# Optimization experiments

Hardware: AMD Instinct MI355X
Metric: run time of the kernel (lower is better)

Reference implementation:

```python
import jax, jax.numpy as jnp
import numpy as np

SIGMA = 5.0            # isotropic, voxel_size = 1 -> sigma_voxel == sigma
TRUNCATE = 3.0         # scipy gaussian_filter default truncate used in source
LABELS = (1, 2, 3, 4, 5, 6, 7, 8)
SHAPE = (128, 128, 128)
# upper-triangle entries of the 3x3 second-moment matrix, in the source's
# sorted order: diagonal (00,11,22) first, then off-diagonals (01,12,02)
XS = np.array([0, 1, 2, 0, 1, 0])
YS = np.array([0, 1, 2, 1, 2, 2])


def _gauss_kernel(sigma):
    r = int(TRUNCATE * sigma + 0.5)
    x = np.arange(-r, r + 1, dtype=np.float32)
    k = np.exp(-0.5 * (x / sigma) ** 2)
    k /= k.sum()
    return jnp.asarray(k, dtype=jnp.float32), r


def _blur_axis(arr, kernel, r, axis):
    # separable 1D convolution along `axis` with zero ('constant', cval=0) padding
    arr = jnp.moveaxis(arr, axis, -1)
    shp = arr.shape
    x = arr.reshape(-1, 1, shp[-1])                      # (N, 1, L)
    out = jax.lax.conv_general_dilated(x, kernel.reshape(1, 1, -1), (1,), [(r, r)])
    return jnp.moveaxis(out.reshape(shp), -1, axis)


def gaussian_blur3d(arr, sigma):
    k, r = _gauss_kernel(sigma)
    for ax in (-3, -2, -1):
        arr = _blur_axis(arr, k, r, ax)
    return arr


def setup_inputs() -> dict:
    key = jax.random.key(0)
    segmentation = jax.random.randint(key, SHAPE, 0, 9, dtype=jnp.int32)
    grid = jnp.meshgrid(*(jnp.arange(s, dtype=jnp.float32) for s in SHAPE), indexing='ij')
    coords = jnp.stack(grid)                              # (3, D, H, W) world coordinates
    return {"segmentation": segmentation, "coords": coords}


def _lsd(segmentation, coords):
    xs = jnp.asarray(XS)
    ys = jnp.asarray(YS)
    acc = jnp.zeros((10,) + SHAPE, dtype=jnp.float32)
    for label in LABELS:                                  # small fixed label set
        mask = (segmentation == label).astype(jnp.float32)        # (D,H,W)
        mc = coords * mask                                        # masked coords (3,...)
        outer = mc[xs] * mc[ys]                                   # unique 2nd moments (6,...)
        stack = jnp.concatenate([mask[None], mc, outer], axis=0)  # (10, D, H, W)
        agg = gaussian_blur3d(stack, SIGMA)                       # fused: one blur for all stats
        mass = agg[0]
        denom = jnp.where(mass > 0, mass, 1.0)                    # safe; invalid voxels masked out below
        com = agg[1:4] / denom                                    # center of mass (3,...)
        # mean offset, normalized by max_distance = sigma, mapped to [0,1]
        mean_offset = ((com - coords) / SIGMA * 0.5 + 0.5) * mask
        cov = (agg[4:10] / denom - com[xs] * com[ys]) / (SIGMA * SIGMA)
        desc = jnp.concatenate([mean_offset, cov, mass[None]], axis=0)
        acc = acc + desc * mask[None]                             # descriptors[mask] += descriptor[mask]
    return jnp.clip(acc, 0.0, 1.0)


def reference(segmentation, coords):
    return _lsd(segmentation, coords)
```

## Files before the change

### kernel.cpp

```cpp
#include <hip/hip_runtime.h>
#include <hip/hip_fp16.h>
#include <math.h>


constexpr int NV = 128 * 128 * 128;
constexpr int SLICE = 128 * 128;
constexpr int R = 15;
constexpr int KL = 31;
constexpr int TS = 6;
constexpr int RSTRIDE = 160 * TS + 8;
constexpr int LCAP = 512;

struct Kw { float k0[KL]; float k1[KL]; float k2[KL]; };

__device__ __forceinline__ void fma4(float4& a, float w, const float4& b) {
    a.x = fmaf(w, b.x, a.x); a.y = fmaf(w, b.y, a.y);
    a.z = fmaf(w, b.z, a.z); a.w = fmaf(w, b.w, a.w);
}

__device__ __forceinline__ float4 load_mask4(const unsigned char* p, int lab) {
    unsigned int u = *(const unsigned int*)p;
    return make_float4(((u       ) & 255u) == (unsigned)lab ? 1.f : 0.f,
                       ((u >>  8 ) & 255u) == (unsigned)lab ? 1.f : 0.f,
                       ((u >> 16 ) & 255u) == (unsigned)lab ? 1.f : 0.f,
                       ((u >> 24 ) & 255u) == (unsigned)lab ? 1.f : 0.f);
}
__device__ __forceinline__ float4 load_mask4(const int* p, int lab) {
    int4 s = *(const int4*)p;
    return make_float4(s.x == lab ? 1.f : 0.f, s.y == lab ? 1.f : 0.f,
                       s.z == lab ? 1.f : 0.f, s.w == lab ? 1.f : 0.f);
}

__device__ __forceinline__ unsigned seg_pack4(const unsigned char* p) {
    return *(const unsigned int*)p;
}
__device__ __forceinline__ unsigned seg_pack4(const int* p) {
    int4 v = *(const int4*)p;
    return (unsigned)(v.x & 255) | ((unsigned)(v.y & 255) << 8) |
           ((unsigned)(v.z & 255) << 16) | ((unsigned)(v.w & 255) << 24);
}

__device__ __forceinline__ unsigned pack_h2(float a, float b) {
    __half2 h = __float22half2_rn(make_float2(a, b));
    return *reinterpret_cast<unsigned*>(&h);
}
__device__ __forceinline__ float h_lo(unsigned u) {
    return __half2float(__ushort_as_half((unsigned short)(u & 0xffffu)));
}
__device__ __forceinline__ float h_hi(unsigned u) {
    return __half2float(__ushort_as_half((unsigned short)(u >> 16)));
}
__device__ __forceinline__ float4 h4_to_f4(uint2 u) {
    return make_float4(h_lo(u.x), h_hi(u.x), h_lo(u.y), h_hi(u.y));
}

template <typename ST>
__global__ __launch_bounds__(256) void pass_z_t(const ST* __restrict__ seg,
                                                unsigned short* __restrict__ A,
                                                int label0, size_t a_stride,
                                                Kw kw) {
    __shared__ float kp[3][37];
    if (threadIdx.x < 37) {
        int i = threadIdx.x, j = i - 3; bool ok = (j >= 0) && (j < KL);
        kp[0][i] = ok ? kw.k0[j] : 0.f;
        kp[1][i] = ok ? kw.k1[j] : 0.f;
        kp[2][i] = ok ? kw.k2[j] : 0.f;
    }
    __syncthreads();
    const int label = label0 + blockIdx.y;
    unsigned short* Ab = A + (size_t)blockIdx.y * a_stride;
    const int h = blockIdx.x, g = h & 7, l = h >> 3;
    const int tx = threadIdx.x & 31, ty = threadIdx.x >> 5;
    const int x0 = tx * 4;
    const int z0 = 16 * g + 4 * (l & 3);
    const int y  = (l >> 2) * 8 + ty;

    float4 acc[4][3];
#pragma unroll
    for (int t = 0; t < 4; ++t)
#pragma unroll
        for (int c = 0; c < 3; ++c) acc[t][c] = make_float4(0.f, 0.f, 0.f, 0.f);

    float4 cm = make_float4(0.f, 0.f, 0.f, 0.f), nm = cm;
    {
        int zz = z0 - R;
        if ((unsigned)zz < 128u)
            cm = load_mask4(seg + (zz * SLICE + y * 128 + x0), label);
        int zn = z0 + 1 - R;
        if ((unsigned)zn < 128u)
            nm = load_mask4(seg + (zn * SLICE + y * 128 + x0), label);
    }
    for (int j = 0; j < 34; ++j) {
        float4 fm = make_float4(0.f, 0.f, 0.f, 0.f);
        int zz = z0 + j + 2 - R;
        if (j < 32 && (unsigned)zz < 128u)
            fm = load_mask4(seg + (zz * SLICE + y * 128 + x0), label);
#pragma unroll
        for (int t = 0; t < 4; ++t) {
            int i = j - t + 3;
            fma4(acc[t][0], kp[0][i], cm);
            fma4(acc[t][1], kp[1][i], cm);
            fma4(acc[t][2], kp[2][i], cm);
        }
        cm = nm; nm = fm;
    }
#pragma unroll
    for (int t = 0; t < 4; ++t) {
        int base = (z0 + t) * SLICE + y * 128 + x0;
#pragma unroll
        for (int c = 0; c < 3; ++c) {
            float4 v = acc[t][c];
            uint2 pv = make_uint2(pack_h2(v.x, v.y), pack_h2(v.z, v.w));
            *reinterpret_cast<uint2*>(Ab + (size_t)c * NV + base) = pv;
        }
    }
}

__device__ __forceinline__ void conv_voxel(const unsigned short* __restrict__ Bu,
                                           int rr, int x, const Kw& kw,
                                           float o[10]) {
    const unsigned short* row = Bu + rr * RSTRIDE + (x + 1) * TS;
    float g000 = 0, g001 = 0, g002 = 0, g010 = 0, g011 = 0,
          g020 = 0, g100 = 0, g101 = 0, g110 = 0, g200 = 0;
#pragma unroll
    for (int j = 0; j < KL; ++j) {
        const unsigned* p = (const unsigned*)(row + TS * j);
        unsigned ua = p[0], ub = p[1], uc = p[2];
        float w0 = kw.k0[j], w1 = kw.k1[j], w2 = kw.k2[j];
        float b0 = h_lo(ua), b1 = h_hi(ua);
        float b2 = h_lo(ub), b3 = h_hi(ub);
        float b4 = h_lo(uc), b5 = h_hi(uc);
        g000 = fmaf(w0, b0, g000); g001 = fmaf(w1, b0, g001); g002 = fmaf(w2, b0, g002);
        g010 = fmaf(w0, b1, g010); g011 = fmaf(w1, b1, g011);
        g020 = fmaf(w0, b2, g020);
        g100 = fmaf(w0, b3, g100); g101 = fmaf(w1, b3, g101);
        g110 = fmaf(w0, b4, g110);
        g200 = fmaf(w0, b5, g200);
    }
    float mass = g000;
    float denom = (mass > 0.f) ? mass : 1.f;
    float inv = 1.f / denom;
    float p = g100 * inv, q = g010 * inv, s = g001 * inv;
    const float cs = 1.0f / 25.0f;
    o[0] = 0.5f - 0.1f * p;
    o[1] = 0.5f - 0.1f * q;
    o[2] = 0.5f - 0.1f * s;
    o[3] = (g200 * inv - p * p) * cs;
    o[4] = (g020 * inv - q * q) * cs;
    o[5] = (g002 * inv - s * s) * cs;
    o[6] = (g110 * inv - p * q) * cs;
    o[7] = (g011 * inv - q * s) * cs;
    o[8] = (g101 * inv - p * s) * cs;
    o[9] = mass;
#pragma unroll
    for (int c = 0; c < 10; ++c) o[c] = fminf(fmaxf(o[c], 0.f), 1.f);
}

__device__ __forceinline__ void do_voxel_out(const unsigned short* __restrict__ Bu,
                                             int rr, int x, int z0, int y0,
                                             float* __restrict__ out, const Kw& kw) {
    float o[10];
    conv_voxel(Bu, rr, x, kw, o);
    const int z2 = z0 + (rr >> 2), y2 = y0 + (rr & 3);
    const int v = (z2 * 128 + y2) * 128 + x;
#pragma unroll
    for (int c = 0; c < 10; ++c) out[(size_t)c * NV + v] = o[c];
}

__device__ __forceinline__ void zero_voxel(int rr, int x, int z0, int y0,
                                           float* __restrict__ out) {
    const int z2 = z0 + (rr >> 2), y2 = y0 + (rr & 3);
    const int v = (z2 * 128 + y2) * 128 + x;
#pragma unroll
    for (int c = 0; c < 10; ++c) out[(size_t)c * NV + v] = 0.f;
}

template <typename ST>
__global__ __launch_bounds__(128) void pass_yx(const unsigned short* __restrict__ A,
                                               const ST* __restrict__ seg,
                                               float* __restrict__ out,
                                               int label0, size_t a_stride,
                                               Kw kw) {
    __shared__ float4 kq4[40];
    __shared__ __align__(16) unsigned short Bu[16 * RSTRIDE];
    __shared__ unsigned short lst[LCAP];
    __shared__ int cnt;

    {
        uint4 z4 = make_uint4(0, 0, 0, 0);
        uint4* b4 = (uint4*)Bu;
        for (int i = threadIdx.x; i < 1936; i += 128) b4[i] = z4;
    }
    if (threadIdx.x < 40) {
        int i = threadIdx.x, j = i - 3; bool ok = (j >= 0) && (j < KL);
        kq4[i] = make_float4(ok ? kw.k0[j] : 0.f, ok ? kw.k1[j] : 0.f,
                             ok ? kw.k2[j] : 0.f, 0.f);
    }
    if (threadIdx.x == 0) cnt = 0;
    __syncthreads();

    const int labi = blockIdx.y;
    const int label = label0 + labi;
    const unsigned short* Ab = A + (size_t)labi * a_stride;
    const int h = blockIdx.x, g = h & 7, l = h >> 3;
    const int tx = threadIdx.x & 31, tz = threadIdx.x >> 5;
    const int x0 = tx * 4;
    const int z0 = 16 * g + 4 * (l & 3);
    const int y0 = (l >> 2) * 4;
    const int zs = (z0 + tz) * SLICE;

    const int rr_c = threadIdx.x >> 3, q0_c = threadIdx.x & 7;
    const int vrow_c = ((z0 + (rr_c >> 2)) * 128 + (y0 + (rr_c & 3))) * 128;
    unsigned pk[4];
#pragma unroll
    for (int k = 0; k < 4; ++k)
        pk[k] = seg_pack4(seg + vrow_c + 4 * (q0_c + 8 * k));

    float4 acc[6][4];
#pragma unroll
    for (int c = 0; c < 6; ++c)
#pragma unroll
        for (int t = 0; t < 4; ++t) acc[c][t] = make_float4(0.f, 0.f, 0.f, 0.f);

    uint2 c0 = make_uint2(0u, 0u), c1 = c0, c2 = c0;
    uint2 n0 = c0, n1 = c0, n2 = c0;
    {
        int yy = y0 - R;
        if ((unsigned)yy < 128u) {
            int base = zs + yy * 128 + x0;
            c0 = *(const uint2*)(Ab + base);
            c1 = *(const uint2*)(Ab + NV + base);
            c2 = *(const uint2*)(Ab + 2 * NV + base);
        }
        int yn = y0 + 1 - R;
        if ((unsigned)yn < 128u) {
            int base = zs + yn * 128 + x0;
            n0 = *(const uint2*)(Ab + base);
            n1 = *(const uint2*)(Ab + NV + base);
            n2 = *(const uint2*)(Ab + 2 * NV + base);
        }
    }
    for (int j = 0; j < 34; ++j) {
        uint2 f0 = make_uint2(0u, 0u), f1 = f0, f2 = f0;
        int yy = y0 + j + 2 - R;
        if (j < 32 && (unsigned)yy < 128u) {
            int base = zs + yy * 128 + x0;
            f0 = *(const uint2*)(Ab + base);
            f1 = *(const uint2*)(Ab + NV + base);
            f2 = *(const uint2*)(Ab + 2 * NV + base);
        }
        float4 a0 = h4_to_f4(c0), a1 = h4_to_f4(c1), a2 = h4_to_f4(c2);
#pragma unroll
        for (int t = 0; t < 4; ++t) {
            float4 wv = kq4[j + 3 - t];
            fma4(acc[0][t], wv.x, a0);
            fma4(acc[1][t], wv.y, a0);
            fma4(acc[2][t], wv.z, a0);
            fma4(acc[3][t], wv.x, a1);
            fma4(acc[4][t], wv.y, a1);
            fma4(acc[5][t], wv.x, a2);
        }
        c0 = n0; c1 = n1; c2 = n2;
        n0 = f0; n1 = f1; n2 = f2;
    }

#pragma unroll
    for (int t = 0; t < 4; ++t) {
        const int row = tz * 4 + t;
        unsigned short* rbase = Bu + row * RSTRIDE + (16 + x0) * TS;
#pragma unroll
        for (int xi = 0; xi < 4; ++xi) {
            unsigned* w32 = (unsigned*)(rbase + xi * TS);
            float v0 = (&acc[0][t].x)[xi], v1 = (&acc[1][t].x)[xi];
            float v2 = (&acc[2][t].x)[xi], v3 = (&acc[3][t].x)[xi];
            float v4 = (&acc[4][t].x)[xi], v5 = (&acc[5][t].x)[xi];
            w32[0] = pack_h2(v0, v1);
            w32[1] = pack_h2(v2, v3);
            w32[2] = pack_h2(v4, v5);
        }
    }

    {
        const int lane = threadIdx.x & 63;
        const unsigned long long below_mask = (1ull << lane) - 1ull;
#pragma unroll
        for (int k = 0; k < 4; ++k) {
            const unsigned w = pk[k];
#pragma unroll
            for (int t = 0; t < 4; ++t) {
                const int sv = (int)((w >> (8 * t)) & 255u);
                const int x = 4 * (q0_c + 8 * k) + t;
                const bool mt = (sv == label);
                const bool zt = !mt && (sv < 1 || sv > 8) &&
                                (((x & 7) + 1) == label);
                const bool pred = mt | zt;
                unsigned long long bal = __ballot(pred);
                int base = 0;
                if (lane == 0 && bal) base = atomicAdd(&cnt, (int)__popcll(bal));
                base = __shfl(base, 0);
                if (pred) {
                    int pos = base + (int)__popcll(bal & below_mask);
                    if (pos < LCAP)
                        lst[pos] = (unsigned short)((rr_c << 7) | x | (zt ? 0x8000 : 0));
                }
            }
        }
    }

    __syncthreads();

    const int total = cnt;
    if (total <= LCAP) {
        for (int e = threadIdx.x; e < total; e += 128) {
            int ent = lst[e];
            int rr = (ent >> 7) & 15, x = ent & 127;
            if (ent & 0x8000) zero_voxel(rr, x, z0, y0, out);
            else do_voxel_out(Bu, rr, x, z0, y0, out, kw);
        }
    } else {
        for (int e = threadIdx.x; e < 2048; e += 128) {
            int rr = e >> 7, x = e & 127;
            int z2 = z0 + (rr >> 2), y2 = y0 + (rr & 3);
            int sv = (int)seg[(z2 * 128 + y2) * 128 + x] & 255;
            if (sv == label)
                do_voxel_out(Bu, rr, x, z0, y0, out, kw);
            else if ((sv < 1 || sv > 8) && (((x & 7) + 1) == label))
                zero_voxel(rr, x, z0, y0, out);
        }
    }
}

__global__ __launch_bounds__(256) void seg_to_u8(const int* __restrict__ seg,
                                                 unsigned char* __restrict__ seg8) {
    const int t = blockIdx.x * 256 + threadIdx.x;
    const int4 s = ((const int4*)seg)[t];
    ((uchar4*)seg8)[t] = make_uchar4((unsigned char)s.x, (unsigned char)s.y,
                                     (unsigned char)s.z, (unsigned char)s.w);
}

extern "C" void kernel_launch(void* const* d_in, const int* in_sizes, int n_in,
                              void* d_out, int out_size, void* d_ws, size_t ws_size,
                              hipStream_t stream) {
    const int* seg = (const int*)d_in[0];
    float* out = (float*)d_out;
    unsigned short* A = (unsigned short*)d_ws;
    const size_t AVOL = (size_t)3 * NV;

    Kw kw;
    double gg[KL], S = 0.0;
    for (int j = 0; j < KL; ++j) { double d = j - R; gg[j] = exp(-0.5 * d * d / 25.0); S += gg[j]; }
    for (int j = 0; j < KL; ++j) {
        double gn = gg[j] / S, d = j - R;
        kw.k0[j] = (float)gn;
        kw.k1[j] = (float)(-d * gn);
        kw.k2[j] = (float)(d * d * gn);
    }


    const size_t need_all = 8 * AVOL * sizeof(unsigned short) + NV;
    const size_t need_one = AVOL * sizeof(unsigned short) + NV;

    if (ws_size >= need_all) {
        unsigned char* seg8 = (unsigned char*)d_ws + 8 * AVOL * sizeof(unsigned short);
        seg_to_u8<<<dim3(2048), dim3(256), 0, stream>>>(seg, seg8);
        pass_z_t<unsigned char><<<dim3(512, 8), dim3(256), 0, stream>>>(
            seg8, A, 1, AVOL, kw);
        pass_yx<unsigned char><<<dim3(1024, 8), dim3(128), 0, stream>>>(
            A, seg8, out, 1, AVOL, kw);
    } else if (ws_size >= need_one) {
        unsigned char* seg8 = (unsigned char*)d_ws + AVOL * sizeof(unsigned short);
        seg_to_u8<<<dim3(2048), dim3(256), 0, stream>>>(seg, seg8);
        for (int label = 1; label <= 8; ++label) {
            pass_z_t<unsigned char><<<dim3(512, 1), dim3(256), 0, stream>>>(
                seg8, A, label, 0, kw);
            pass_yx<unsigned char><<<dim3(1024, 1), dim3(128), 0, stream>>>(
                A, seg8, out, label, 0, kw);
        }
    } else {
        for (int label = 1; label <= 8; ++label) {
            pass_z_t<int><<<dim3(512, 1), dim3(256), 0, stream>>>(
                seg, A, label, 0, kw);
            pass_yx<int><<<dim3(1024, 1), dim3(128), 0, stream>>>(
                A, seg, out, label, 0, kw);
        }
    }
}
```

Before: 408.8 us.

## Use planar shared-memory layout and fully unrolled z/y convolutions with register weights

Changes the shared staging buffer from interleaved six-channel voxels to planar per-channel rows, so writes become packed uint2 stores and the x-convolution reads scalar halves per channel. Fully unrolls the z and y convolution loops and reads kernel weights straight from the kernel-argument struct instead of shared-memory tables, which removes the rotating register pipeline and the LDS weight loads. Shrinks the list capacity. The cost is more code, higher register pressure, and 16-bit LDS loads in the inner x loop instead of 32-bit paired loads.

```diff
diff --git a/kernel.cpp b/kernel.cpp
--- a/kernel.cpp
+++ b/kernel.cpp
@@ -7,9 +7,9 @@
 constexpr int SLICE = 128 * 128;
 constexpr int R = 15;
 constexpr int KL = 31;
-constexpr int TS = 6;
-constexpr int RSTRIDE = 160 * TS + 8;
-constexpr int LCAP = 512;
+constexpr int CSTRIDE = 160;
+constexpr int RSTRIDE = 6 * CSTRIDE + 8;
+constexpr int LCAP = 320;
 
 struct Kw { float k0[KL]; float k1[KL]; float k2[KL]; };
 
@@ -44,14 +44,14 @@
     __half2 h = __float22half2_rn(make_float2(a, b));
     return *reinterpret_cast<unsigned*>(&h);
 }
-__device__ __forceinline__ float h_lo(unsigned u) {
-    return __half2float(__ushort_as_half((unsigned short)(u & 0xffffu)));
-}
-__device__ __forceinline__ float h_hi(unsigned u) {
-    return __half2float(__ushort_as_half((unsigned short)(u >> 16)));
+__device__ __forceinline__ float hf_ld(const unsigned short* p) {
+    return __half2float(__ushort_as_half(*p));
 }
 __device__ __forceinline__ float4 h4_to_f4(uint2 u) {
-    return make_float4(h_lo(u.x), h_hi(u.x), h_lo(u.y), h_hi(u.y));
+    return make_float4(__half2float(__ushort_as_half((unsigned short)(u.x & 0xffffu))),
+                       __half2float(__ushort_as_half((unsigned short)(u.x >> 16))),
+                       __half2float(__ushort_as_half((unsigned short)(u.y & 0xffffu))),
+                       __half2float(__ushort_as_half((unsigned short)(u.y >> 16))));
 }
 
 template <typename ST>
@@ -59,14 +59,6 @@
                                                 unsigned short* __restrict__ A,
                                                 int label0, size_t a_stride,
                                                 Kw kw) {
-    __shared__ float kp[3][37];
-    if (threadIdx.x < 37) {
-        int i = threadIdx.x, j = i - 3; bool ok = (j >= 0) && (j < KL);
-        kp[0][i] = ok ? kw.k0[j] : 0.f;
-        kp[1][i] = ok ? kw.k1[j] : 0.f;
-        kp[2][i] = ok ? kw.k2[j] : 0.f;
-    }
-    __syncthreads();
     const int label = label0 + blockIdx.y;
     unsigned short* Ab = A + (size_t)blockIdx.y * a_stride;
     const int h = blockIdx.x, g = h & 7, l = h >> 3;
@@ -81,28 +73,21 @@
 #pragma unroll
         for (int c = 0; c < 3; ++c) acc[t][c] = make_float4(0.f, 0.f, 0.f, 0.f);
 
-    float4 cm = make_float4(0.f, 0.f, 0.f, 0.f), nm = cm;
-    {
-        int zz = z0 - R;
+#pragma unroll
+    for (int j = 0; j < 34; ++j) {
+        float4 m = make_float4(0.f, 0.f, 0.f, 0.f);
+        int zz = z0 + j - R;
         if ((unsigned)zz < 128u)
-            cm = load_mask4(seg + (zz * SLICE + y * 128 + x0), label);
-        int zn = z0 + 1 - R;
-        if ((unsigned)zn < 128u)
-            nm = load_mask4(seg + (zn * SLICE + y * 128 + x0), label);
-    }
-    for (int j = 0; j < 34; ++j) {
-        float4 fm = make_float4(0.f, 0.f, 0.f, 0.f);
-        int zz = z0 + j + 2 - R;
-        if (j < 32 && (unsigned)zz < 128u)
-            fm = load_mask4(seg + (zz * SLICE + y * 128 + x0), label);
+            m = load_mask4(seg + (zz * SLICE + y * 128 + x0), label);
 #pragma unroll
         for (int t = 0; t < 4; ++t) {
-            int i = j - t + 3;
-            fma4(acc[t][0], kp[0][i], cm);
-            fma4(acc[t][1], kp[1][i], cm);
-            fma4(acc[t][2], kp[2][i], cm);
-        }
-        cm = nm; nm = fm;
+            const int idx = j - t;
+            if (idx >= 0 && idx < KL) {
+                fma4(acc[t][0], kw.k0[idx], m);
+                fma4(acc[t][1], kw.k1[idx], m);
+                fma4(acc[t][2], kw.k2[idx], m);
+            }
+        }
     }
 #pragma unroll
     for (int t = 0; t < 4; ++t) {
@@ -119,17 +104,18 @@
 __device__ __forceinline__ void conv_voxel(const unsigned short* __restrict__ Bu,
                                            int rr, int x, const Kw& kw,
                                            float o[10]) {
-    const unsigned short* row = Bu + rr * RSTRIDE + (x + 1) * TS;
+    const unsigned short* row = Bu + rr * RSTRIDE + (x + 1);
     float g000 = 0, g001 = 0, g002 = 0, g010 = 0, g011 = 0,
           g020 = 0, g100 = 0, g101 = 0, g110 = 0, g200 = 0;
 #pragma unroll
     for (int j = 0; j < KL; ++j) {
-        const unsigned* p = (const unsigned*)(row + TS * j);
-        unsigned ua = p[0], ub = p[1], uc = p[2];
         float w0 = kw.k0[j], w1 = kw.k1[j], w2 = kw.k2[j];
-        float b0 = h_lo(ua), b1 = h_hi(ua);
-        float b2 = h_lo(ub), b3 = h_hi(ub);
-        float b4 = h_lo(uc), b5 = h_hi(uc);
+        float b0 = hf_ld(row + 0 * CSTRIDE + j);
+        float b1 = hf_ld(row + 1 * CSTRIDE + j);
+        float b2 = hf_ld(row + 2 * CSTRIDE + j);
+        float b3 = hf_ld(row + 3 * CSTRIDE + j);
+        float b4 = hf_ld(row + 4 * CSTRIDE + j);
+        float b5 = hf_ld(row + 5 * CSTRIDE + j);
         g000 = fmaf(w0, b0, g000); g001 = fmaf(w1, b0, g001); g002 = fmaf(w2, b0, g002);
         g010 = fmaf(w0, b1, g010); g011 = fmaf(w1, b1, g011);
         g020 = fmaf(w0, b2, g020);
@@ -181,7 +167,6 @@
                                                float* __restrict__ out,
                                                int label0, size_t a_stride,
                                                Kw kw) {
-    __shared__ float4 kq4[40];
     __shared__ __align__(16) unsigned short Bu[16 * RSTRIDE];
     __shared__ unsigned short lst[LCAP];
     __shared__ int cnt;
@@ -190,11 +175,6 @@
         uint4 z4 = make_uint4(0, 0, 0, 0);
         uint4* b4 = (uint4*)Bu;
         for (int i = threadIdx.x; i < 1936; i += 128) b4[i] = z4;
-    }
-    if (threadIdx.x < 40) {
-        int i = threadIdx.x, j = i - 3; bool ok = (j >= 0) && (j < KL);
-        kq4[i] = make_float4(ok ? kw.k0[j] : 0.f, ok ? kw.k1[j] : 0.f,
-                             ok ? kw.k2[j] : 0.f, 0.f);
     }
     if (threadIdx.x == 0) cnt = 0;
     __syncthreads();
@@ -222,61 +202,40 @@
 #pragma unroll
         for (int t = 0; t < 4; ++t) acc[c][t] = make_float4(0.f, 0.f, 0.f, 0.f);
 
-    uint2 c0 = make_uint2(0u, 0u), c1 = c0, c2 = c0;
-    uint2 n0 = c0, n1 = c0, n2 = c0;
-    {
-        int yy = y0 - R;
+#pragma unroll
+    for (int j = 0; j < 34; ++j) {
+        uint2 u0 = make_uint2(0u, 0u), u1 = u0, u2 = u0;
+        int yy = y0 + j - R;
         if ((unsigned)yy < 128u) {
             int base = zs + yy * 128 + x0;
-            c0 = *(const uint2*)(Ab + base);
-            c1 = *(const uint2*)(Ab + NV + base);
-            c2 = *(const uint2*)(Ab + 2 * NV + base);
-        }
-        int yn = y0 + 1 - R;
-        if ((unsigned)yn < 128u) {
-            int base = zs + yn * 128 + x0;
-            n0 = *(const uint2*)(Ab + base);
-            n1 = *(const uint2*)(Ab + NV + base);
-            n2 = *(const uint2*)(Ab + 2 * NV + base);
-        }
-    }
-    for (int j = 0; j < 34; ++j) {
-        uint2 f0 = make_uint2(0u, 0u), f1 = f0, f2 = f0;
-        int yy = y0 + j + 2 - R;
-        if (j < 32 && (unsigned)yy < 128u) {
-            int base = zs + yy * 128 + x0;
-            f0 = *(const uint2*)(Ab + base);
-            f1 = *(const uint2*)(Ab + NV + base);
-            f2 = *(const uint2*)(Ab + 2 * NV + base);
-        }
-        float4 a0 = h4_to_f4(c0), a1 = h4_to_f4(c1), a2 = h4_to_f4(c2);
+            u0 = *(const uint2*)(Ab + base);
+            u1 = *(const uint2*)(Ab + NV + base);
+            u2 = *(const uint2*)(Ab + 2 * NV + base);
+        }
+        float4 a0 = h4_to_f4(u0), a1 = h4_to_f4(u1), a2 = h4_to_f4(u2);
 #pragma unroll
         for (int t = 0; t < 4; ++t) {
-            float4 wv = kq4[j + 3 - t];
-            fma4(acc[0][t], wv.x, a0);
-            fma4(acc[1][t], wv.y, a0);
-            fma4(acc[2][t], wv.z, a0);
-            fma4(acc[3][t], wv.x, a1);
-            fma4(acc[4][t], wv.y, a1);
-            fma4(acc[5][t], wv.x, a2);
-        }
-        c0 = n0; c1 = n1; c2 = n2;
-        n0 = f0; n1 = f1; n2 = f2;
+            const int idx = j - t;
+            if (idx >= 0 && idx < KL) {
+                float w0 = kw.k0[idx], w1 = kw.k1[idx], w2 = kw.k2[idx];
+                fma4(acc[0][t], w0, a0);
+                fma4(acc[1][t], w1, a0);
+                fma4(acc[2][t], w2, a0);
+                fma4(acc[3][t], w0, a1);
+                fma4(acc[4][t], w1, a1);
+                fma4(acc[5][t], w0, a2);
+            }
+        }
     }
 
 #pragma unroll
     for (int t = 0; t < 4; ++t) {
         const int row = tz * 4 + t;
-        unsigned short* rbase = Bu + row * RSTRIDE + (16 + x0) * TS;
-#pragma unroll
-        for (int xi = 0; xi < 4; ++xi) {
-            unsigned* w32 = (unsigned*)(rbase + xi * TS);
-            float v0 = (&acc[0][t].x)[xi], v1 = (&acc[1][t].x)[xi];
-            float v2 = (&acc[2][t].x)[xi], v3 = (&acc[3][t].x)[xi];
-            float v4 = (&acc[4][t].x)[xi], v5 = (&acc[5][t].x)[xi];
-            w32[0] = pack_h2(v0, v1);
-            w32[1] = pack_h2(v2, v3);
-            w32[2] = pack_h2(v4, v5);
+#pragma unroll
+        for (int c = 0; c < 6; ++c) {
+            uint2 pv = make_uint2(pack_h2(acc[c][t].x, acc[c][t].y),
+                                  pack_h2(acc[c][t].z, acc[c][t].w));
+            *reinterpret_cast<uint2*>(Bu + row * RSTRIDE + c * CSTRIDE + 16 + x0) = pv;
         }
     }
 
```

Result: slower. 657.0 us (+60.7%).
